# Optimization experiments

Hardware: AMD Instinct MI355X
Metric: run time of the kernel (lower is better)

The kernel has to match this reference:

```python
import jax, jax.numpy as jnp
import numpy as np

SEQ, B, IN, H, OUT = 600, 4096, 6, 30, 61


def setup_inputs() -> dict:
    key = jax.random.key(0)
    ks = jax.random.split(key, 9)
    s_ih = 1.0 / np.sqrt(H)
    return {
        "X": jax.random.normal(ks[0], (SEQ, B, IN), dtype=jnp.float32),
        "W_ih": jax.random.uniform(ks[1], (4 * H, IN), jnp.float32, -s_ih, s_ih),
        "W_hh": jax.random.uniform(ks[2], (4 * H, H), jnp.float32, -s_ih, s_ih),
        "b_ih": jax.random.uniform(ks[3], (4 * H,), jnp.float32, -s_ih, s_ih),
        "b_hh": jax.random.uniform(ks[4], (4 * H,), jnp.float32, -s_ih, s_ih),
        "W1": jax.random.uniform(ks[5], (H, H), jnp.float32, -s_ih, s_ih),
        "b1": jax.random.uniform(ks[6], (H,), jnp.float32, -s_ih, s_ih),
        "W2": jax.random.uniform(ks[7], (OUT, H), jnp.float32, -s_ih, s_ih),
        "b2": jax.random.uniform(ks[8], (OUT,), jnp.float32, -s_ih, s_ih),
        "batch_size": B,
    }


def _lstm_last_h(X, W_ih, W_hh, b_ih, b_hh):
    # Precompute input projections for all timesteps: [T, B, 4H]
    xg = jnp.einsum("tbi,gi->tbg", X, W_ih) + b_ih + b_hh
    h0 = jnp.zeros((X.shape[1], W_hh.shape[1]), X.dtype)
    c0 = jnp.zeros_like(h0)

    def step(carry, xg_t):
        h, c = carry
        g = xg_t + h @ W_hh.T  # [B, 4H]
        i, f, gg, o = jnp.split(g, 4, axis=-1)  # PyTorch gate order i,f,g,o
        c = jax.nn.sigmoid(f) * c + jax.nn.sigmoid(i) * jnp.tanh(gg)
        h = jax.nn.sigmoid(o) * jnp.tanh(c)
        return (h, c), None

    (h, _), _ = jax.lax.scan(step, (h0, c0), xg)
    return h  # out[-1, :, :]


def reference(X, W_ih, W_hh, b_ih, b_hh, W1, b1, W2, b2, batch_size):
    h = _lstm_last_h(X, W_ih, W_hh, b_ih, b_hh)
    out = h @ W1.T + b1  # fc1
    # dropout(p=0.6) is identity in eval mode
    out = out @ W2.T + b2  # fc2
    return out  # [B, 61]
```

## Files before the change

### kernel.cpp

```cpp
#include <hip/hip_runtime.h>


#define SEQ    600
#define BATCH  4096
#define INP    6
#define HID    30
#define NOUT   61
#define LOG2E  1.4426950408889634f
#define LOG2E2 2.8853900817779268f

typedef __fp16 f16;
typedef f16  f16x2 __attribute__((ext_vector_type(2)));
typedef f16  f16x8 __attribute__((ext_vector_type(8)));
typedef float f32x2 __attribute__((ext_vector_type(2)));
typedef float f32x4 __attribute__((ext_vector_type(4)));

__device__ __forceinline__ float rcp_(float x)  { return __builtin_amdgcn_rcpf(x); }
__device__ __forceinline__ float exp2_(float x) { return __builtin_amdgcn_exp2f(x); }
__device__ __forceinline__ unsigned cvtpk(float a, float b) {
    union { f16x2 h; unsigned u; } c;
    c.h = __builtin_amdgcn_cvt_pkrtz(a, b);
    return c.u;
}
__device__ __forceinline__ f16x8 mk8(unsigned a, unsigned b, unsigned c, unsigned d) {
    union { unsigned u[4]; f16x8 v; } x;
    x.u[0] = a; x.u[1] = b; x.u[2] = c; x.u[3] = d;
    return x.v;
}
__device__ __forceinline__ float asf(int u) {
    union { int i; float f; } c; c.i = u; return c.f;
}
__device__ __forceinline__ int asi(float f) {
    union { float f; int i; } c; c.f = f; return c.i;
}
__device__ __forceinline__ float sigm_(float x) {
    return rcp_(1.0f + exp2_(-LOG2E * x));
}
__device__ __forceinline__ float tanh_(float x) {
    return fmaf(-2.0f, rcp_(exp2_(LOG2E2 * x) + 1.0f), 1.0f);
}

extern "C" __global__ void __launch_bounds__(64, 1)
lstm_m5(const float* __restrict__ X,   const float* __restrict__ Wih,
        const float* __restrict__ Whh, const float* __restrict__ bih,
        const float* __restrict__ bhh, const float* __restrict__ W1,
        const float* __restrict__ b1,  const float* __restrict__ W2,
        const float* __restrict__ b2,  float* __restrict__ out)
{
    __shared__ float h32[4][32];
    __shared__ float o1s[4][32];

    const int l  = threadIdx.x;
    const int g  = l >> 4;
    const int n  = l & 15;
    const int e  = n & 3;
    const int j  = n >> 2;
    const int e0 = blockIdx.x * 4;
    const bool jb0 = (j & 1) != 0;
    const bool jb1 = (j & 2) != 0;
    const bool isg3 = (g == 3);

    f16x8 Ah[8], Ax[8];
    {
        const int q = n & 3;
        #pragma unroll
        for (int m = 0; m < 8; ++m) {
            const int u  = 4 * m + (n >> 2);
            const bool ov = (u < HID);
            const int row = q * HID + (ov ? u : 0);
            unsigned dh[4], dx[4];
            #pragma unroll
            for (int jp = 0; jp < 4; ++jp) {
                const int k0 = 8 * g + 2 * jp, k1 = k0 + 1;
                float v0 = (ov && k0 < HID) ? Whh[row * HID + k0] : 0.f;
                float v1 = (ov && k1 < HID) ? Whh[row * HID + k1]
                         : ((ov && k1 == 31) ? (bih[row] + bhh[row]) : 0.f);
                dh[jp] = cvtpk(v0, v1);
                float w0 = (ov && k0 < INP) ? Wih[row * INP + k0] : 0.f;
                float w1 = (ov && k1 < INP) ? Wih[row * INP + k1] : 0.f;
                dx[jp] = cvtpk(w0, w1);
            }
            Ah[m] = mk8(dh[0], dh[1], dh[2], dh[3]);
            Ax[m] = mk8(dx[0], dx[1], dx[2], dx[3]);
        }
    }

    const int A0 = (4 * g + e) * 4;
    const int A1 = (16 + 4 * g + e) * 4;
    const int A2 = (32 + 4 * g + e) * 4;
    const int A3 = (48 + 4 * g + e) * 4;

    const float* xsrc = X + (size_t)(e0 + e) * INP;

    float cA = 0.f, cB = 0.f;
    float hA = 0.f, hB = 0.f;

    f32x2 xq0, xq1, xq2;
    { const float* p = xsrc; xq0 = *(const f32x2*)p; xq1 = *(const f32x2*)(p+2); xq2 = *(const f32x2*)(p+4); }

    f32x4 xcA[8], xcB[8];
    const f32x4 ZZ = {0.f, 0.f, 0.f, 0.f};

    #define XACC(DST) do {                                                     \
        const unsigned c0 = cvtpk(xq0.x, xq0.y);                               \
        const unsigned c1 = cvtpk(xq1.x, xq1.y);                               \
        const unsigned c2 = cvtpk(xq2.x, xq2.y);                               \
        const f16x8 Bx = mk8(g == 0 ? c0 : 0u, g == 0 ? c1 : 0u,               \
                             g == 0 ? c2 : 0u, 0u);                            \
        _Pragma("unroll")                                                      \
        for (int m = 0; m < 8; ++m)                                            \
            DST[m] = __builtin_amdgcn_mfma_f32_16x16x32_f16(Ax[m], Bx, ZZ, 0, 0, 0); \
    } while (0)

    XACC(xcA);
    { const float* p = xsrc + (size_t)BATCH * INP;
      xq0 = *(const f32x2*)p; xq1 = *(const f32x2*)(p+2); xq2 = *(const f32x2*)(p+4); }

    #define ITER(XC, XN, T) do {                                               \
                         \
        const int r0 = __builtin_amdgcn_ds_bpermute(A0, asi(hA));              \
        const int r1 = __builtin_amdgcn_ds_bpermute(A1, asi(hA));              \
        const int r2 = __builtin_amdgcn_ds_bpermute(A2, asi(hA));              \
        const int r3 = __builtin_amdgcn_ds_bpermute(A3, asi(hA));              \
        const int r4 = __builtin_amdgcn_ds_bpermute(A0, asi(hB));              \
        const int r5 = __builtin_amdgcn_ds_bpermute(A1, asi(hB));              \
        const int r6 = __builtin_amdgcn_ds_bpermute(A2, asi(hB));              \
        const int r7 = __builtin_amdgcn_ds_bpermute(A3, asi(hB));              \
        const unsigned dw0 = cvtpk(asf(r0), asf(r1));                          \
        const unsigned dw1 = cvtpk(asf(r2), asf(r3));                          \
        const unsigned dw2 = cvtpk(asf(r4), asf(r5));                          \
        unsigned dw3 = cvtpk(asf(r6), asf(r7));                                \
        dw3 = isg3 ? 0x3C000000u : dw3;        \
        const f16x8 Bh = mk8(dw0, dw1, dw2, dw3);                              \
        f32x4 C[8];                                                            \
        _Pragma("unroll")                                                      \
        for (int m = 0; m < 8; ++m)                                            \
            C[m] = __builtin_amdgcn_mfma_f32_16x16x32_f16(Ah[m], Bh, XC[m], 0, 0, 0); \
        \
        XACC(XN);                                                              \
                                               \
        { int tt = (T) + 2; if (tt > SEQ - 1) tt = SEQ - 1;                    \
          const float* p = xsrc + (size_t)tt * BATCH * INP;                    \
          xq0 = *(const f32x2*)p; xq1 = *(const f32x2*)(p+2);                  \
          xq2 = *(const f32x2*)(p+4); }                                        \
                \
        const f32x4 sA0 = jb0 ? C[2] : C[0];                                   \
        const f32x4 sA1 = jb0 ? C[6] : C[4];                                   \
        const f32x4 GA  = jb1 ? sA1 : sA0;                                     \
        const f32x4 sB0 = jb0 ? C[3] : C[1];                                   \
        const f32x4 sB1 = jb0 ? C[7] : C[5];                                   \
        const f32x4 GB  = jb1 ? sB1 : sB0;                                     \
                                                \
        const float siA = sigm_(GA.x), sfA = sigm_(GA.y);                      \
        const float tgA = tanh_(GA.z), soA = sigm_(GA.w);                      \
        const float siB = sigm_(GB.x), sfB = sigm_(GB.y);                      \
        const float tgB = tanh_(GB.z), soB = sigm_(GB.w);                      \
        cA = fmaf(sfA, cA, siA * tgA);                                         \
        cB = fmaf(sfB, cB, siB * tgB);                                         \
        hA = soA * tanh_(cA);                                                  \
        hB = soB * tanh_(cB);                                                  \
    } while (0)

    for (int t = 0; t < SEQ; t += 2) {
        ITER(xcA, xcB, t);
        ITER(xcB, xcA, t + 1);
    }
    #undef ITER
    #undef XACC

    h32[e][8 * j + g]     = hA;
    h32[e][8 * j + 4 + g] = hB;
    asm volatile("s_waitcnt lgkmcnt(0)" ::: "memory");

    {
        float hr[HID];
        #pragma unroll
        for (int k = 0; k < HID; ++k) hr[k] = h32[g][k];
        float a0 = b1[n];
        const float* w1r0 = W1 + n * HID;
        #pragma unroll
        for (int k = 0; k < HID; ++k) a0 = fmaf(w1r0[k], hr[k], a0);
        o1s[g][n] = a0;
        if (n < 14) {
            float a1 = b1[n + 16];
            const float* w1r1 = W1 + (n + 16) * HID;
            #pragma unroll
            for (int k = 0; k < HID; ++k) a1 = fmaf(w1r1[k], hr[k], a1);
            o1s[g][n + 16] = a1;
        }
    }
    asm volatile("s_waitcnt lgkmcnt(0)" ::: "memory");

    {
        float orr[HID];
        #pragma unroll
        for (int k = 0; k < HID; ++k) orr[k] = o1s[g][k];
        #pragma unroll
        for (int r = 0; r < 4; ++r) {
            const int o = n + 16 * r;
            if (o < NOUT) {
                float a2 = b2[o];
                const float* w2r = W2 + o * HID;
                #pragma unroll
                for (int k = 0; k < HID; ++k) a2 = fmaf(w2r[k], orr[k], a2);
                out[(size_t)(e0 + g) * NOUT + o] = a2;
            }
        }
    }
}

extern "C" void kernel_launch(void* const* d_in, const int* in_sizes, int n_in,
                              void* d_out, int out_size, void* d_ws, size_t ws_size,
                              hipStream_t stream) {
    const float* X   = (const float*)d_in[0];
    const float* Wih = (const float*)d_in[1];
    const float* Whh = (const float*)d_in[2];
    const float* bih = (const float*)d_in[3];
    const float* bhh = (const float*)d_in[4];
    const float* W1  = (const float*)d_in[5];
    const float* b1  = (const float*)d_in[6];
    const float* W2  = (const float*)d_in[7];
    const float* b2  = (const float*)d_in[8];
    float* out = (float*)d_out;

    dim3 grid(BATCH / 4);
    dim3 block(64);
    hipLaunchKernelGGL(lstm_m5, grid, block, 0, stream,
                       X, Wih, Whh, bih, bhh, W1, b1, W2, b2, out);
}
```

Measured before the change: 370.8 us.

## Halve batch elements per block to double resident waves per SIMD

Each 64-lane block now processes 2 batch elements instead of 4, so the grid doubles and launch bounds allow two waves per SIMD. Each lane carries one cell/hidden state instead of two, which shortens the serial gate-activation chain per step. Operand gathering and gate selection are remapped, with an extra select level. The intent is to hide the latency of the recurrent dependency chain by interleaving two waves per SIMD. The cost is that total MFMA and bpermute work doubles, because each MFMA now carries half as many useful batch columns.

Measured after the change: 345.1 us. 1.07x faster.

```diff
diff --git a/kernel.cpp b/kernel.cpp
--- a/kernel.cpp
+++ b/kernel.cpp
@@ -40,24 +40,25 @@
     return fmaf(-2.0f, rcp_(exp2_(LOG2E2 * x) + 1.0f), 1.0f);
 }
 
-extern "C" __global__ void __launch_bounds__(64, 1)
-lstm_m5(const float* __restrict__ X,   const float* __restrict__ Wih,
+extern "C" __global__ void __launch_bounds__(64, 2)
+lstm_m6(const float* __restrict__ X,   const float* __restrict__ Wih,
         const float* __restrict__ Whh, const float* __restrict__ bih,
         const float* __restrict__ bhh, const float* __restrict__ W1,
         const float* __restrict__ b1,  const float* __restrict__ W2,
         const float* __restrict__ b2,  float* __restrict__ out)
 {
-    __shared__ float h32[4][32];
-    __shared__ float o1s[4][32];
+    __shared__ float h32[2][32];
+    __shared__ float o1s[2][32];
 
     const int l  = threadIdx.x;
     const int g  = l >> 4;
     const int n  = l & 15;
-    const int e  = n & 3;
-    const int j  = n >> 2;
-    const int e0 = blockIdx.x * 4;
+    const int e  = n & 1;
+    const int j  = n >> 1;
+    const int e0 = blockIdx.x * 2;
     const bool jb0 = (j & 1) != 0;
     const bool jb1 = (j & 2) != 0;
+    const bool jb2 = (j & 4) != 0;
     const bool isg3 = (g == 3);
 
     f16x8 Ah[8], Ax[8];
@@ -89,11 +90,14 @@
     const int A1 = (16 + 4 * g + e) * 4;
     const int A2 = (32 + 4 * g + e) * 4;
     const int A3 = (48 + 4 * g + e) * 4;
+    const int A4 = (4 * g + 2 + e) * 4;
+    const int A5 = (16 + 4 * g + 2 + e) * 4;
+    const int A6 = (32 + 4 * g + 2 + e) * 4;
+    const int A7 = (48 + 4 * g + 2 + e) * 4;
 
     const float* xsrc = X + (size_t)(e0 + e) * INP;
 
-    float cA = 0.f, cB = 0.f;
-    float hA = 0.f, hB = 0.f;
+    float c = 0.f, h = 0.f;
 
     f32x2 xq0, xq1, xq2;
     { const float* p = xsrc; xq0 = *(const f32x2*)p; xq1 = *(const f32x2*)(p+2); xq2 = *(const f32x2*)(p+4); }
@@ -117,15 +121,15 @@
       xq0 = *(const f32x2*)p; xq1 = *(const f32x2*)(p+2); xq2 = *(const f32x2*)(p+4); }
 
     #define ITER(XC, XN, T) do {                                               \
-                         \
-        const int r0 = __builtin_amdgcn_ds_bpermute(A0, asi(hA));              \
-        const int r1 = __builtin_amdgcn_ds_bpermute(A1, asi(hA));              \
-        const int r2 = __builtin_amdgcn_ds_bpermute(A2, asi(hA));              \
-        const int r3 = __builtin_amdgcn_ds_bpermute(A3, asi(hA));              \
-        const int r4 = __builtin_amdgcn_ds_bpermute(A0, asi(hB));              \
-        const int r5 = __builtin_amdgcn_ds_bpermute(A1, asi(hB));              \
-        const int r6 = __builtin_amdgcn_ds_bpermute(A2, asi(hB));              \
-        const int r7 = __builtin_amdgcn_ds_bpermute(A3, asi(hB));              \
+                             \
+        const int r0 = __builtin_amdgcn_ds_bpermute(A0, asi(h));               \
+        const int r1 = __builtin_amdgcn_ds_bpermute(A1, asi(h));               \
+        const int r2 = __builtin_amdgcn_ds_bpermute(A2, asi(h));               \
+        const int r3 = __builtin_amdgcn_ds_bpermute(A3, asi(h));               \
+        const int r4 = __builtin_amdgcn_ds_bpermute(A4, asi(h));               \
+        const int r5 = __builtin_amdgcn_ds_bpermute(A5, asi(h));               \
+        const int r6 = __builtin_amdgcn_ds_bpermute(A6, asi(h));               \
+        const int r7 = __builtin_amdgcn_ds_bpermute(A7, asi(h));               \
         const unsigned dw0 = cvtpk(asf(r0), asf(r1));                          \
         const unsigned dw1 = cvtpk(asf(r2), asf(r3));                          \
         const unsigned dw2 = cvtpk(asf(r4), asf(r5));                          \
@@ -143,22 +147,19 @@
           const float* p = xsrc + (size_t)tt * BATCH * INP;                    \
           xq0 = *(const f32x2*)p; xq1 = *(const f32x2*)(p+2);                  \
           xq2 = *(const f32x2*)(p+4); }                                        \
-                \
-        const f32x4 sA0 = jb0 ? C[2] : C[0];                                   \
-        const f32x4 sA1 = jb0 ? C[6] : C[4];                                   \
-        const f32x4 GA  = jb1 ? sA1 : sA0;                                     \
-        const f32x4 sB0 = jb0 ? C[3] : C[1];                                   \
-        const f32x4 sB1 = jb0 ? C[7] : C[5];                                   \
-        const f32x4 GB  = jb1 ? sB1 : sB0;                                     \
-                                                \
-        const float siA = sigm_(GA.x), sfA = sigm_(GA.y);                      \
-        const float tgA = tanh_(GA.z), soA = sigm_(GA.w);                      \
-        const float siB = sigm_(GB.x), sfB = sigm_(GB.y);                      \
-        const float tgB = tanh_(GB.z), soB = sigm_(GB.w);                      \
-        cA = fmaf(sfA, cA, siA * tgA);                                         \
-        cB = fmaf(sfB, cB, siB * tgB);                                         \
-        hA = soA * tanh_(cA);                                                  \
-        hB = soB * tanh_(cB);                                                  \
+               \
+        const f32x4 s0 = jb0 ? C[1] : C[0];                                    \
+        const f32x4 s1 = jb0 ? C[3] : C[2];                                    \
+        const f32x4 s2 = jb0 ? C[5] : C[4];                                    \
+        const f32x4 s3 = jb0 ? C[7] : C[6];                                    \
+        const f32x4 t0 = jb1 ? s1 : s0;                                        \
+        const f32x4 t1 = jb1 ? s3 : s2;                                        \
+        const f32x4 G  = jb2 ? t1 : t0;                                        \
+                               \
+        const float si = sigm_(G.x), sf = sigm_(G.y);                          \
+        const float tg = tanh_(G.z), so = sigm_(G.w);                          \
+        c = fmaf(sf, c, si * tg);                                              \
+        h = so * tanh_(c);                                                     \
     } while (0)
 
     for (int t = 0; t < SEQ; t += 2) {
@@ -168,42 +169,32 @@
     #undef ITER
     #undef XACC
 
-    h32[e][8 * j + g]     = hA;
-    h32[e][8 * j + 4 + g] = hB;
+    h32[e][4 * j + g] = h;
     asm volatile("s_waitcnt lgkmcnt(0)" ::: "memory");
 
     {
-        float hr[HID];
-        #pragma unroll
-        for (int k = 0; k < HID; ++k) hr[k] = h32[g][k];
-        float a0 = b1[n];
-        const float* w1r0 = W1 + n * HID;
-        #pragma unroll
-        for (int k = 0; k < HID; ++k) a0 = fmaf(w1r0[k], hr[k], a0);
-        o1s[g][n] = a0;
-        if (n < 14) {
-            float a1 = b1[n + 16];
-            const float* w1r1 = W1 + (n + 16) * HID;
+        const int half = l >> 5;
+        const int u    = l & 31;
+        if (u < HID) {
+            float a1 = b1[u];
+            const float* w1r = W1 + u * HID;
             #pragma unroll
-            for (int k = 0; k < HID; ++k) a1 = fmaf(w1r1[k], hr[k], a1);
-            o1s[g][n + 16] = a1;
+            for (int k = 0; k < HID; ++k) a1 = fmaf(w1r[k], h32[half][k], a1);
+            o1s[half][u] = a1;
         }
     }
     asm volatile("s_waitcnt lgkmcnt(0)" ::: "memory");
 
     {
-        float orr[HID];
-        #pragma unroll
-        for (int k = 0; k < HID; ++k) orr[k] = o1s[g][k];
-        #pragma unroll
-        for (int r = 0; r < 4; ++r) {
-            const int o = n + 16 * r;
-            if (o < NOUT) {
+        const int half = l >> 5;
+        const int u    = l & 31;
+        if (u < HID) {
+            for (int o = u; o < NOUT; o += HID) {
                 float a2 = b2[o];
                 const float* w2r = W2 + o * HID;
                 #pragma unroll
-                for (int k = 0; k < HID; ++k) a2 = fmaf(w2r[k], orr[k], a2);
-                out[(size_t)(e0 + g) * NOUT + o] = a2;
+                for (int k = 0; k < HID; ++k) a2 = fmaf(w2r[k], o1s[half][k], a2);
+                out[(size_t)(e0 + half) * NOUT + o] = a2;
             }
         }
     }
@@ -223,8 +214,8 @@
     const float* b2  = (const float*)d_in[8];
     float* out = (float*)d_out;
 
-    dim3 grid(BATCH / 4);
+    dim3 grid(BATCH / 2);
     dim3 block(64);
-    hipLaunchKernelGGL(lstm_m5, grid, block, 0, stream,
+    hipLaunchKernelGGL(lstm_m6, grid, block, 0, stream,
                        X, Wih, Whh, bih, bhh, W1, b1, W2, b2, out);
 }
```
